# Kernel tuning notes

Measured on AMD Instinct MI355X. Metric: run time of the kernel, lower is better.

## Reference

```python
import jax, jax.numpy as jnp
import numpy as np

B, N, K = 1, 1024, 4
E = N * K  # 4096
FV, FE, NH, FOUT = 512, 64, 256, 250


def _sym_norm(a):
    d = a.sum(1)
    di = jnp.where(d > 0, 1.0 / jnp.sqrt(d), 0.0)
    return a * di[:, None] * di[None, :]


def setup_inputs() -> dict:
    key = jax.random.key(0)
    ks = jax.random.split(key, 12)
    # random k-NN style edge pairs (B, N, K, 2)
    ep = jax.random.randint(ks[0], (B, N, K, 2), 0, N)
    s = ep[..., 0].reshape(B, E)
    e = ep[..., 1].reshape(B, E)
    cols = jnp.arange(E)

    def build_T(sb, eb):  # incidence / transition matrix (N, E), duplicates summed
        return jnp.zeros((N, E), jnp.float32).at[sb, cols].add(1.0).at[eb, cols].add(1.0)

    T = jax.vmap(build_T)(s, e)

    def build_adj_e(sb, eb):  # edges adjacent iff they share an endpoint
        m = ((sb[:, None] == sb[None, :]) | (sb[:, None] == eb[None, :]) |
             (eb[:, None] == sb[None, :]) | (eb[:, None] == eb[None, :])).astype(jnp.float32)
        return _sym_norm(m + jnp.eye(E, dtype=jnp.float32))  # plus_one normalize

    adj_e = jax.vmap(build_adj_e)(s, e)

    def build_adj_v(sb, eb):
        a = jnp.zeros((N, N), jnp.float32).at[sb, eb].set(1.0).at[eb, sb].set(1.0)
        return _sym_norm(a)

    adj_v = jax.vmap(build_adj_v)(s, e)

    X = jax.random.normal(ks[1], (B, N, FV), jnp.float32)
    Z = jax.random.normal(ks[2], (B, E, FE), jnp.float32)

    def unif(k, shape, fan_out):  # matches reset_parameters: U(-1/sqrt(out), 1/sqrt(out))
        st = 1.0 / np.sqrt(fan_out)
        return jax.random.uniform(k, shape, jnp.float32, -st, st)

    w1 = unif(ks[3], (FV, NH), NH); b1 = unif(ks[4], (NH,), NH)
    p1 = jax.random.normal(ks[5], (1, FE), jnp.float32)
    w2 = unif(ks[6], (FE, 2 * FE), 2 * FE); b2 = unif(ks[7], (2 * FE,), 2 * FE)
    p2 = jax.random.normal(ks[8], (1, NH), jnp.float32)
    w3 = unif(ks[9], (NH, FOUT), FOUT); b3 = unif(ks[10], (FOUT,), FOUT)
    p3 = jax.random.normal(ks[11], (1, 2 * FE), jnp.float32)
    return dict(X=X, Z=Z, adj_e=adj_e, adj_v=adj_v, T=T,
                w1=w1, p1=p1, b1=b1, w2=w2, p2=p2, b2=b2, w3=w3, p3=p3, b3=b3)


def _node_layer(Hv, He, av, Tb, W, p, bias):
    v = (He @ p.T)[:, 0]                                   # (E,) edge scores
    mult = jnp.einsum('ne,e,me->nm', Tb, v, Tb)            # T diag(v) T^T, (N, N)
    eye = jnp.eye(mult.shape[0], dtype=mult.dtype)
    A = (eye + (1.0 - eye) * mult) * av                    # eye-blend then adj mask
    # NOTE: original computes GELU(output) but then overwrites it with output + bias
    # whenever bias is present (bias=True here), so the activation is discarded.
    return A @ (Hv @ W) + bias


def _edge_layer(Hv, He, ae, Tb, W, p, bias):
    v = (Hv @ p.T)[:, 0]                                   # (N,) node scores
    mult = jnp.einsum('ne,n,nf->ef', Tb, v, Tb)            # T^T diag(v) T, (E, E)
    eye = jnp.eye(mult.shape[0], dtype=mult.dtype)
    A = (eye + (1.0 - eye) * mult) * ae
    A = A / jnp.max(A, axis=0, keepdims=True)              # column-max normalize
    return A @ (He @ W) + bias


def reference(X, Z, adj_e, adj_v, T, w1, p1, b1, w2, p2, b2, w3, p3, b3):
    def single(Hv, He, ae, av, Tb):
        x = jax.nn.relu(_node_layer(Hv, He, av, Tb, w1, p1, b1))  # gc1 (node)
        z = jax.nn.relu(He)
        z = jax.nn.relu(_edge_layer(x, z, ae, Tb, w2, p2, b2))    # gc2 (edge)
        x = _node_layer(x, z, av, Tb, w3, p3, b3)                 # gc3 (node)
        return x, z
    return jax.vmap(single)(X, Z, adj_e, adj_v, T)  # dropout p=0 / eval mode
```

## Files before the change

kernel.cpp:

```cpp
#include <hip/hip_runtime.h>

#define NN 1024
#define NE 4096
#define FVD 512
#define FED 64
#define NHD 256
#define FOUTD 250
#define ICAP 64
#define VCAP 64
#define ECAP 128

__global__ __launch_bounds__(256) void scan_T(
    const float* __restrict__ T, int* __restrict__ se, int* __restrict__ te) {
  size_t i = (size_t)blockIdx.x * blockDim.x + threadIdx.x;
  if (i >= (size_t)NN * NE) return;
  float v = T[i];
  if (v > 0.5f) {
    int n = (int)(i >> 12);
    int e = (int)(i & (NE - 1));
    atomicMin(&se[e], n);
    atomicMax(&te[e], n);
  }
}

__global__ __launch_bounds__(256) void build_inc(
    int* __restrict__ se, int* __restrict__ te,
    int* __restrict__ inc, int* __restrict__ icnt) {
  int e = blockIdx.x * blockDim.x + threadIdx.x;
  if (e >= NE) return;
  int s = se[e], t = te[e];
  if (s < 0 || s >= NN) { s = 0; se[e] = 0; }
  if (t < 0 || t >= NN) { t = s; te[e] = s; }
  int p = atomicAdd(&icnt[s], 1);
  if (p < ICAP) inc[s * ICAP + p] = e;
  if (t != s) {
    p = atomicAdd(&icnt[t], 1);
    if (p < ICAP) inc[t * ICAP + p] = e;
  }
}

__global__ void compact_rows(const float* __restrict__ A, int R, int C, int cap,
                             int* __restrict__ cols, float* __restrict__ vals,
                             float* __restrict__ diag, int* __restrict__ cnt) {
  int wid = (blockIdx.x * blockDim.x + threadIdx.x) >> 6;
  int lane = threadIdx.x & 63;
  if (wid >= R) return;
  const float4* row = (const float4*)(A + (size_t)wid * C);
  int base = 0;
  for (int c0 = 0; c0 < C; c0 += 256) {
    float4 v4 = row[(c0 >> 2) + lane];
    float vv[4] = {v4.x, v4.y, v4.z, v4.w};
    #pragma unroll
    for (int j = 0; j < 4; j++) {
      int c = c0 + lane * 4 + j;
      float v = vv[j];
      if (c == wid) diag[wid] = v;
      bool pred = (v != 0.0f) && (c != wid);
      unsigned long long m = __ballot(pred);
      if (pred) {
        int idx = base + __popcll(m & ((1ull << lane) - 1ull));
        if (idx < cap) {
          cols[(size_t)wid * cap + idx] = c;
          vals[(size_t)wid * cap + idx] = v;
        }
      }
      base += __popcll(m);
    }
  }
  if (lane == 0) cnt[wid] = base < cap ? base : cap;
}

__global__ void wave_dot(const float* __restrict__ X, const float* __restrict__ p,
                         float* __restrict__ out, int rows, int D) {
  int wid = (blockIdx.x * blockDim.x + threadIdx.x) >> 6;
  int lane = threadIdx.x & 63;
  if (wid >= rows) return;
  float acc = 0.0f;
  for (int d = lane; d < D; d += 64) acc += X[(size_t)wid * D + d] * p[d];
  for (int off = 32; off; off >>= 1) acc += __shfl_down(acc, off);
  if (lane == 0) out[wid] = acc;
}

template <bool RELU_A>
__global__ __launch_bounds__(256) void gemm32(const float* __restrict__ A,
                                              const float* __restrict__ B,
                                              float* __restrict__ C,
                                              int M, int N, int K) {
  __shared__ float As[32][33];
  __shared__ float Bs[32][33];
  int tid = threadIdx.x;
  int tx = tid & 15, ty = tid >> 4;
  int bm = blockIdx.y * 32, bn = blockIdx.x * 32;
  float acc00 = 0.f, acc01 = 0.f, acc10 = 0.f, acc11 = 0.f;
  for (int k0 = 0; k0 < K; k0 += 32) {
    for (int i = tid; i < 32 * 32; i += 256) {
      int r = i >> 5, c = i & 31;
      int gr = bm + r, gc = k0 + c;
      float v = (gr < M && gc < K) ? A[(size_t)gr * K + gc] : 0.f;
      if (RELU_A) v = fmaxf(v, 0.f);
      As[r][c] = v;
    }
    for (int i = tid; i < 32 * 32; i += 256) {
      int r = i >> 5, c = i & 31;
      int gr = k0 + r, gc = bn + c;
      Bs[r][c] = (gr < K && gc < N) ? B[(size_t)gr * N + gc] : 0.f;
    }
    __syncthreads();
    #pragma unroll
    for (int kk = 0; kk < 32; kk++) {
      float a0 = As[ty * 2][kk], a1 = As[ty * 2 + 1][kk];
      float b0 = Bs[kk][tx * 2], b1 = Bs[kk][tx * 2 + 1];
      acc00 += a0 * b0; acc01 += a0 * b1;
      acc10 += a1 * b0; acc11 += a1 * b1;
    }
    __syncthreads();
  }
  int r0 = bm + ty * 2, c0 = bn + tx * 2;
  if (r0 < M) {
    if (c0 < N) C[(size_t)r0 * N + c0] = acc00;
    if (c0 + 1 < N) C[(size_t)r0 * N + c0 + 1] = acc01;
  }
  if (r0 + 1 < M) {
    if (c0 < N) C[(size_t)(r0 + 1) * N + c0] = acc10;
    if (c0 + 1 < N) C[(size_t)(r0 + 1) * N + c0 + 1] = acc11;
  }
}

template <bool RELU>
__global__ __launch_bounds__(256) void node_apply(
    const float* __restrict__ HW, int H, const float* __restrict__ v,
    const int* __restrict__ se, const int* __restrict__ te,
    const int* __restrict__ inc, const int* __restrict__ icnt,
    const int* __restrict__ avc, const float* __restrict__ avv,
    const float* __restrict__ avd, const int* __restrict__ avcnt,
    const float* __restrict__ bias, float* __restrict__ out) {
  int n = blockIdx.x;
  __shared__ float scoef[VCAP];
  __shared__ int scol[VCAP];
  int cnt = avcnt[n];
  int tid = threadIdx.x;
  if (tid < cnt) {
    int m = avc[n * VCAP + tid];
    float mult = 0.0f;
    int ic = icnt[n]; if (ic > ICAP) ic = ICAP;
    for (int k = 0; k < ic; k++) {
      int e = inc[n * ICAP + k];
      int s = se[e], t = te[e];
      float wn = (float)((s == n) + (t == n));
      float wm = (float)((s == m) + (t == m));
      mult += wn * v[e] * wm;
    }
    scoef[tid] = mult * avv[n * VCAP + tid];
    scol[tid] = m;
  }
  __syncthreads();
  float d = avd[n];
  for (int h = tid; h < H; h += 256) {
    float acc = d * HW[(size_t)n * H + h];
    for (int k = 0; k < cnt; k++)
      acc += scoef[k] * HW[(size_t)scol[k] * H + h];
    acc += bias[h];
    if (RELU) acc = fmaxf(acc, 0.0f);
    out[(size_t)n * H + h] = acc;
  }
}

__global__ __launch_bounds__(256) void edge_coef(
    const float* __restrict__ v2, const int* __restrict__ se, const int* __restrict__ te,
    const int* __restrict__ aec, const float* __restrict__ aev,
    const float* __restrict__ aed, const int* __restrict__ aecnt,
    float* __restrict__ coef, float* __restrict__ rmax) {
  int i = blockIdx.x * blockDim.x + threadIdx.x;
  if (i >= NE) return;
  int s = se[i], t = te[i];
  float vs = v2[s], vt = v2[t];
  int cnt = aecnt[i];
  float mx = aed[i];
  for (int k = 0; k < cnt; k++) {
    int j = aec[i * ECAP + k];
    int sj = se[j], tj = te[j];
    float m;
    if (s == t) {
      m = 2.0f * vs * (float)((sj == s) + (tj == s));
    } else {
      m = vs * (float)((sj == s) + (tj == s)) + vt * (float)((sj == t) + (tj == t));
    }
    float c = m * aev[i * ECAP + k];
    coef[i * ECAP + k] = c;
    mx = fmaxf(mx, c);
  }
  rmax[i] = mx;
}

__global__ __launch_bounds__(128) void edge_apply(
    const float* __restrict__ ZW, const int* __restrict__ aec,
    const float* __restrict__ coef, const float* __restrict__ aed,
    const int* __restrict__ aecnt, const float* __restrict__ rmax,
    const float* __restrict__ bias, float* __restrict__ out) {
  int i = blockIdx.x;
  int h = threadIdx.x;
  __shared__ float sw[ECAP];
  __shared__ int sj[ECAP];
  int cnt = aecnt[i];
  if (h < cnt) {
    int j = aec[i * ECAP + h];
    sj[h] = j;
    sw[h] = coef[i * ECAP + h] / rmax[j];
  }
  __syncthreads();
  float acc = (aed[i] / rmax[i]) * ZW[(size_t)i * 128 + h];
  for (int k = 0; k < cnt; k++)
    acc += sw[k] * ZW[(size_t)sj[k] * 128 + h];
  acc += bias[h];
  out[(size_t)i * 128 + h] = fmaxf(acc, 0.0f);
}

extern "C" void kernel_launch(void* const* d_in, const int* in_sizes, int n_in,
                              void* d_out, int out_size, void* d_ws, size_t ws_size,
                              hipStream_t stream) {
  const float* X    = (const float*)d_in[0];
  const float* Z    = (const float*)d_in[1];
  const float* adjE = (const float*)d_in[2];
  const float* adjV = (const float*)d_in[3];
  const float* T    = (const float*)d_in[4];
  const float* w1   = (const float*)d_in[5];
  const float* p1   = (const float*)d_in[6];
  const float* b1   = (const float*)d_in[7];
  const float* w2   = (const float*)d_in[8];
  const float* p2   = (const float*)d_in[9];
  const float* b2   = (const float*)d_in[10];
  const float* w3   = (const float*)d_in[11];
  const float* p3   = (const float*)d_in[12];
  const float* b3   = (const float*)d_in[13];

  float* xout = (float*)d_out;
  float* zout = xout + (size_t)NN * FOUTD;

  char* w = (char*)d_ws;
  auto alloc = [&](size_t bytes) {
    char* p = w;
    w += (bytes + 255) & ~(size_t)255;
    return p;
  };
  int*   se    = (int*)alloc(NE * 4);
  int*   te    = (int*)alloc(NE * 4);
  int*   icnt  = (int*)alloc(NN * 4);
  int*   inc   = (int*)alloc((size_t)NN * ICAP * 4);
  int*   avc   = (int*)alloc((size_t)NN * VCAP * 4);
  float* avv   = (float*)alloc((size_t)NN * VCAP * 4);
  float* avd   = (float*)alloc(NN * 4);
  int*   avcnt = (int*)alloc(NN * 4);
  int*   aec   = (int*)alloc((size_t)NE * ECAP * 4);
  float* aev   = (float*)alloc((size_t)NE * ECAP * 4);
  float* aed   = (float*)alloc(NE * 4);
  int*   aecnt = (int*)alloc(NE * 4);
  float* coef2 = (float*)alloc((size_t)NE * ECAP * 4);
  float* rmax  = (float*)alloc(NE * 4);
  float* v1    = (float*)alloc(NE * 4);
  float* v2    = (float*)alloc(NN * 4);
  float* v3    = (float*)alloc(NE * 4);
  float* HW1   = (float*)alloc((size_t)NN * NHD * 4);
  float* x1    = (float*)alloc((size_t)NN * NHD * 4);
  float* ZW2   = (float*)alloc((size_t)NE * 128 * 4);
  float* XW3   = (float*)alloc((size_t)NN * FOUTD * 4);
  (void)ws_size; (void)in_sizes; (void)n_in; (void)out_size;

  hipMemsetAsync(icnt, 0, NN * 4, stream);
  hipMemsetAsync(se, 0x7f, NE * 4, stream);
  hipMemsetAsync(te, 0xff, NE * 4, stream);

  scan_T<<<(NN * NE) / 256, 256, 0, stream>>>(T, se, te);
  build_inc<<<NE / 256, 256, 0, stream>>>(se, te, inc, icnt);
  compact_rows<<<NN * 64 / 256, 256, 0, stream>>>(adjV, NN, NN, VCAP, avc, avv, avd, avcnt);
  compact_rows<<<NE * 64 / 256, 256, 0, stream>>>(adjE, NE, NE, ECAP, aec, aev, aed, aecnt);

  wave_dot<<<NE * 64 / 256, 256, 0, stream>>>(Z, p1, v1, NE, FED);
  {
    dim3 g((NHD + 31) / 32, (NN + 31) / 32);
    gemm32<false><<<g, 256, 0, stream>>>(X, w1, HW1, NN, NHD, FVD);
  }
  node_apply<true><<<NN, 256, 0, stream>>>(HW1, NHD, v1, se, te, inc, icnt,
                                           avc, avv, avd, avcnt, b1, x1);

  wave_dot<<<NN * 64 / 256, 256, 0, stream>>>(x1, p2, v2, NN, NHD);
  {
    dim3 g((128 + 31) / 32, (NE + 31) / 32);
    gemm32<true><<<g, 256, 0, stream>>>(Z, w2, ZW2, NE, 128, FED);
  }
  edge_coef<<<NE / 256, 256, 0, stream>>>(v2, se, te, aec, aev, aed, aecnt, coef2, rmax);
  edge_apply<<<NE, 128, 0, stream>>>(ZW2, aec, coef2, aed, aecnt, rmax, b2, zout);

  wave_dot<<<NE * 64 / 256, 256, 0, stream>>>(zout, p3, v3, NE, 128);
  {
    dim3 g((FOUTD + 31) / 32, (NN + 31) / 32);
    gemm32<false><<<g, 256, 0, stream>>>(x1, w3, XW3, NN, FOUTD, NHD);
  }
  node_apply<false><<<NN, 256, 0, stream>>>(XW3, FOUTD, v3, se, te, inc, icnt,
                                            avc, avv, avd, avcnt, b3, xout);
}
```

Before: 308.2 us.

## Replace shared-memory GEMM with float4 register-tiled split-K GEMM plus reduction

Replaces the 32x32 LDS-tiled GEMM with a register-blocked kernel. Each thread computes 4 rows by a float4 of output columns, reading B as float4 directly from global memory with no shared memory or barriers. The K dimension is split across blockIdx.y into partial buffers, and a separate reduce kernel sums them. w3 is padded to 256 columns so every GEMM width is a multiple of 4. This adds partial-buffer traffic and extra launches in exchange for more parallelism and vectorized loads on these small GEMMs.

```diff
diff --git a/kernel.cpp b/kernel.cpp
--- a/kernel.cpp
+++ b/kernel.cpp
@@ -81,54 +81,72 @@
   if (lane == 0) out[wid] = acc;
 }
 
-template <bool RELU_A>
-__global__ __launch_bounds__(256) void gemm32(const float* __restrict__ A,
-                                              const float* __restrict__ B,
-                                              float* __restrict__ C,
-                                              int M, int N, int K) {
-  __shared__ float As[32][33];
-  __shared__ float Bs[32][33];
+template <bool RELU_A, int N4, int KK, int KSPLIT>
+__global__ __launch_bounds__(256) void gemm_f4(
+    const float* __restrict__ A, const float* __restrict__ B,
+    float* __restrict__ Cpart, int M) {
+  constexpr int RPT = 4;
+  constexpr int RG = 256 / N4;
+  constexpr int KPS = KK / KSPLIT;
   int tid = threadIdx.x;
-  int tx = tid & 15, ty = tid >> 4;
-  int bm = blockIdx.y * 32, bn = blockIdx.x * 32;
-  float acc00 = 0.f, acc01 = 0.f, acc10 = 0.f, acc11 = 0.f;
-  for (int k0 = 0; k0 < K; k0 += 32) {
-    for (int i = tid; i < 32 * 32; i += 256) {
-      int r = i >> 5, c = i & 31;
-      int gr = bm + r, gc = k0 + c;
-      float v = (gr < M && gc < K) ? A[(size_t)gr * K + gc] : 0.f;
-      if (RELU_A) v = fmaxf(v, 0.f);
-      As[r][c] = v;
-    }
-    for (int i = tid; i < 32 * 32; i += 256) {
-      int r = i >> 5, c = i & 31;
-      int gr = k0 + r, gc = bn + c;
-      Bs[r][c] = (gr < K && gc < N) ? B[(size_t)gr * N + gc] : 0.f;
-    }
-    __syncthreads();
+  int c4 = tid % N4;
+  int rg = tid / N4;
+  int ks = blockIdx.y;
+  int m0 = blockIdx.x * (RG * RPT) + rg * RPT;
+  const float4* B4 = (const float4*)B;
+  float4 acc[RPT];
+  #pragma unroll
+  for (int r = 0; r < RPT; r++) acc[r] = make_float4(0.f, 0.f, 0.f, 0.f);
+  int kbeg = ks * KPS;
+  #pragma unroll 4
+  for (int kc = 0; kc < KPS; kc += 4) {
+    int k = kbeg + kc;
+    float4 b0 = B4[(size_t)(k + 0) * N4 + c4];
+    float4 b1 = B4[(size_t)(k + 1) * N4 + c4];
+    float4 b2 = B4[(size_t)(k + 2) * N4 + c4];
+    float4 b3 = B4[(size_t)(k + 3) * N4 + c4];
     #pragma unroll
-    for (int kk = 0; kk < 32; kk++) {
-      float a0 = As[ty * 2][kk], a1 = As[ty * 2 + 1][kk];
-      float b0 = Bs[kk][tx * 2], b1 = Bs[kk][tx * 2 + 1];
-      acc00 += a0 * b0; acc01 += a0 * b1;
-      acc10 += a1 * b0; acc11 += a1 * b1;
-    }
-    __syncthreads();
-  }
-  int r0 = bm + ty * 2, c0 = bn + tx * 2;
-  if (r0 < M) {
-    if (c0 < N) C[(size_t)r0 * N + c0] = acc00;
-    if (c0 + 1 < N) C[(size_t)r0 * N + c0 + 1] = acc01;
-  }
-  if (r0 + 1 < M) {
-    if (c0 < N) C[(size_t)(r0 + 1) * N + c0] = acc10;
-    if (c0 + 1 < N) C[(size_t)(r0 + 1) * N + c0 + 1] = acc11;
-  }
+    for (int r = 0; r < RPT; r++) {
+      float4 a = *(const float4*)(A + (size_t)(m0 + r) * KK + k);
+      if (RELU_A) {
+        a.x = fmaxf(a.x, 0.f); a.y = fmaxf(a.y, 0.f);
+        a.z = fmaxf(a.z, 0.f); a.w = fmaxf(a.w, 0.f);
+      }
+      acc[r].x += a.x * b0.x; acc[r].y += a.x * b0.y; acc[r].z += a.x * b0.z; acc[r].w += a.x * b0.w;
+      acc[r].x += a.y * b1.x; acc[r].y += a.y * b1.y; acc[r].z += a.y * b1.z; acc[r].w += a.y * b1.w;
+      acc[r].x += a.z * b2.x; acc[r].y += a.z * b2.y; acc[r].z += a.z * b2.z; acc[r].w += a.z * b2.w;
+      acc[r].x += a.w * b3.x; acc[r].y += a.w * b3.y; acc[r].z += a.w * b3.z; acc[r].w += a.w * b3.w;
+    }
+  }
+  float4* out = (float4*)Cpart + ((size_t)ks * M + m0) * N4 + c4;
+  #pragma unroll
+  for (int r = 0; r < RPT; r++) out[(size_t)r * N4] = acc[r];
+}
+
+__global__ void reduce_part(const float4* __restrict__ part, float4* __restrict__ out,
+                            int n4, int ksplit) {
+  int i = blockIdx.x * blockDim.x + threadIdx.x;
+  int stride = gridDim.x * blockDim.x;
+  for (; i < n4; i += stride) {
+    float4 s = part[i];
+    for (int k = 1; k < ksplit; k++) {
+      float4 p = part[(size_t)k * n4 + i];
+      s.x += p.x; s.y += p.y; s.z += p.z; s.w += p.w;
+    }
+    out[i] = s;
+  }
+}
+
+__global__ void pad_w3(const float* __restrict__ w3, float* __restrict__ w3p) {
+  int i = blockIdx.x * blockDim.x + threadIdx.x;
+  if (i >= 256 * 256) return;
+  int r = i >> 8, c = i & 255;
+  w3p[i] = (c < FOUTD) ? w3[r * FOUTD + c] : 0.f;
 }
 
 template <bool RELU>
 __global__ __launch_bounds__(256) void node_apply(
-    const float* __restrict__ HW, int H, const float* __restrict__ v,
+    const float* __restrict__ HW, int H, int ldH, const float* __restrict__ v,
     const int* __restrict__ se, const int* __restrict__ te,
     const int* __restrict__ inc, const int* __restrict__ icnt,
     const int* __restrict__ avc, const float* __restrict__ avv,
@@ -156,9 +174,9 @@
   __syncthreads();
   float d = avd[n];
   for (int h = tid; h < H; h += 256) {
-    float acc = d * HW[(size_t)n * H + h];
+    float acc = d * HW[(size_t)n * ldH + h];
     for (int k = 0; k < cnt; k++)
-      acc += scoef[k] * HW[(size_t)scol[k] * H + h];
+      acc += scoef[k] * HW[(size_t)scol[k] * ldH + h];
     acc += bias[h];
     if (RELU) acc = fmaxf(acc, 0.0f);
     out[(size_t)n * H + h] = acc;
@@ -262,7 +280,9 @@
   float* HW1   = (float*)alloc((size_t)NN * NHD * 4);
   float* x1    = (float*)alloc((size_t)NN * NHD * 4);
   float* ZW2   = (float*)alloc((size_t)NE * 128 * 4);
-  float* XW3   = (float*)alloc((size_t)NN * FOUTD * 4);
+  float* XW3p  = (float*)alloc((size_t)NN * 256 * 4);
+  float* w3p   = (float*)alloc(256 * 256 * 4);
+  float* gpart = (float*)alloc((size_t)8 * NN * NHD * 4);
   (void)ws_size; (void)in_sizes; (void)n_in; (void)out_size;
 
   hipMemsetAsync(icnt, 0, NN * 4, stream);
@@ -273,28 +293,26 @@
   build_inc<<<NE / 256, 256, 0, stream>>>(se, te, inc, icnt);
   compact_rows<<<NN * 64 / 256, 256, 0, stream>>>(adjV, NN, NN, VCAP, avc, avv, avd, avcnt);
   compact_rows<<<NE * 64 / 256, 256, 0, stream>>>(adjE, NE, NE, ECAP, aec, aev, aed, aecnt);
+  pad_w3<<<256, 256, 0, stream>>>(w3, w3p);
 
   wave_dot<<<NE * 64 / 256, 256, 0, stream>>>(Z, p1, v1, NE, FED);
-  {
-    dim3 g((NHD + 31) / 32, (NN + 31) / 32);
-    gemm32<false><<<g, 256, 0, stream>>>(X, w1, HW1, NN, NHD, FVD);
-  }
-  node_apply<true><<<NN, 256, 0, stream>>>(HW1, NHD, v1, se, te, inc, icnt,
+  gemm_f4<false, 64, 512, 8><<<dim3(64, 8), 256, 0, stream>>>(X, w1, gpart, NN);
+  reduce_part<<<512, 256, 0, stream>>>((const float4*)gpart, (float4*)HW1,
+                                       NN * NHD / 4, 8);
+  node_apply<true><<<NN, 256, 0, stream>>>(HW1, NHD, NHD, v1, se, te, inc, icnt,
                                            avc, avv, avd, avcnt, b1, x1);
 
   wave_dot<<<NN * 64 / 256, 256, 0, stream>>>(x1, p2, v2, NN, NHD);
-  {
-    dim3 g((128 + 31) / 32, (NE + 31) / 32);
-    gemm32<true><<<g, 256, 0, stream>>>(Z, w2, ZW2, NE, 128, FED);
-  }
+  gemm_f4<true, 32, 64, 4><<<dim3(128, 4), 256, 0, stream>>>(Z, w2, gpart, NE);
+  reduce_part<<<512, 256, 0, stream>>>((const float4*)gpart, (float4*)ZW2,
+                                       NE * 128 / 4, 4);
   edge_coef<<<NE / 256, 256, 0, stream>>>(v2, se, te, aec, aev, aed, aecnt, coef2, rmax);
   edge_apply<<<NE, 128, 0, stream>>>(ZW2, aec, coef2, aed, aecnt, rmax, b2, zout);
 
   wave_dot<<<NE * 64 / 256, 256, 0, stream>>>(zout, p3, v3, NE, 128);
-  {
-    dim3 g((FOUTD + 31) / 32, (NN + 31) / 32);
-    gemm32<false><<<g, 256, 0, stream>>>(x1, w3, XW3, NN, FOUTD, NHD);
-  }
-  node_apply<false><<<NN, 256, 0, stream>>>(XW3, FOUTD, v3, se, te, inc, icnt,
+  gemm_f4<false, 64, 256, 8><<<dim3(64, 8), 256, 0, stream>>>(x1, w3p, gpart, NN);
+  reduce_part<<<512, 256, 0, stream>>>((const float4*)gpart, (float4*)XW3p,
+                                       NN * 256 / 4, 8);
+  node_apply<false><<<NN, 256, 0, stream>>>(XW3p, FOUTD, 256, v3, se, te, inc, icnt,
                                             avc, avv, avd, avcnt, b3, xout);
 }
```

New measurement: 266.4 us. 13.6% less time.
